# Optimization experiments

Measured on AMD Instinct MI355X. Metric: run time of the kernel, lower is better.

The kernel has to match this reference:

```python
import jax, jax.numpy as jnp
import numpy as np

V, D, B, S = 32000, 1024, 4, 2048
EPS = 1e-12  # matches torch F.normalize eps


def setup_inputs() -> dict:
    key = jax.random.key(0)
    k1, k2, k3 = jax.random.split(key, 3)
    init_embed = jax.random.normal(k1, (V, D), dtype=jnp.float32)
    scale = np.sqrt(D).astype(np.float32)  # default scale = sqrt(embed_dim)
    norm = jnp.maximum(jnp.linalg.norm(init_embed, axis=-1, keepdims=True), EPS)
    in_weight = scale * (init_embed / norm)            # [V, D]
    out_weight = init_embed.T                          # [D, V]
    inputs = jax.random.randint(k2, (B, S), 0, V)      # token ids
    embeds = jax.random.normal(k3, (B, S, D), dtype=jnp.float32)
    return {"inputs": inputs, "embeds": embeds, "in_weight": in_weight, "out_weight": out_weight}


def reference(inputs, embeds, in_weight, out_weight):
    # embed(): one_hot @ in_weight is mathematically an index gather
    embedded = jnp.take(in_weight, inputs, axis=0)          # [B, S, D]
    # unembed(): dense matmul against transposed embedding table
    logits = jnp.einsum('bsd,dv->bsv', embeds, out_weight)  # [B, S, V]
    return embedded, logits
```

## Files before the change

kernel.cpp:

```cpp
#include <hip/hip_runtime.h>
#include <hip/hip_bf16.h>
#include <stdint.h>

#define V_SZ 32000
#define D_SZ 1024
#define M_SZ 8192

typedef __attribute__((ext_vector_type(8))) short bf16x8;
typedef __attribute__((ext_vector_type(4))) float f32x4;
typedef __attribute__((ext_vector_type(16))) float f32x16;

static __device__ __forceinline__ unsigned short f32_to_bf16_rne(float f) {
    union { float f; uint32_t u; } v; v.f = f;
    uint32_t u = v.u;
    uint32_t lsb = (u >> 16) & 1;
    u += 0x7fffu + lsb;
    return (unsigned short)(u >> 16);
}

__global__ void gather_rows(const int* __restrict__ ids,
                            const float* __restrict__ table,
                            float* __restrict__ out) {
    int row = blockIdx.x;
    int id  = ids[row];
    const f32x4* src = (const f32x4*)(table + (size_t)id * D_SZ);
    f32x4*       dst = (f32x4*)(out + (size_t)row * D_SZ);
    __builtin_nontemporal_store(src[threadIdx.x], &dst[threadIdx.x]);
}

__global__ void cast_f32_bf16(const float* __restrict__ in,
                              unsigned short* __restrict__ out, int n8) {
    int i = blockIdx.x * blockDim.x + threadIdx.x;
    int stride = gridDim.x * blockDim.x;
    for (; i < n8; i += stride) {
        const float4* p = (const float4*)(in + (size_t)i * 8);
        float4 a = p[0], b = p[1];
        union { unsigned short s[8]; uint4 v; } r;
        r.s[0] = f32_to_bf16_rne(a.x); r.s[1] = f32_to_bf16_rne(a.y);
        r.s[2] = f32_to_bf16_rne(a.z); r.s[3] = f32_to_bf16_rne(a.w);
        r.s[4] = f32_to_bf16_rne(b.x); r.s[5] = f32_to_bf16_rne(b.y);
        r.s[6] = f32_to_bf16_rne(b.z); r.s[7] = f32_to_bf16_rne(b.w);
        ((uint4*)out)[i] = r.v;
    }
}

__global__ void transpose_cast(const float* __restrict__ w,
                               unsigned short* __restrict__ bt) {
    __shared__ unsigned short tile[32][34];
    int n0 = blockIdx.x * 32;
    int k0 = blockIdx.y * 32;
    int r = threadIdx.x >> 5;
    int c = threadIdx.x & 31;
#pragma unroll
    for (int rr = 0; rr < 32; rr += 8) {
        float v = w[(size_t)(k0 + r + rr) * V_SZ + (n0 + c)];
        tile[c][r + rr] = f32_to_bf16_rne(v);
    }
    __syncthreads();
    int nl = threadIdx.x >> 3;
    int ks = threadIdx.x & 7;
    union { unsigned short s[4]; uint2 v; } r2;
#pragma unroll
    for (int j = 0; j < 4; ++j) r2.s[j] = tile[nl][ks * 4 + j];
    ((uint2*)(bt + (size_t)(n0 + nl) * D_SZ + k0))[ks] = r2.v;
}

#define BM 256
#define BN 256
#define BK 64
#define NSTEP (D_SZ / BK)

static __device__ __forceinline__ void gload_lds16(const unsigned short* g, void* lds) {
    __builtin_amdgcn_global_load_lds(
        (const __attribute__((address_space(1))) void*)g,
        (__attribute__((address_space(3))) void*)lds,
        16, 0, 0);
}

__global__ __launch_bounds__(512, 2)
void gemm_persist(const unsigned short* __restrict__ A,
                  const unsigned short* __restrict__ Bt,
                  float* __restrict__ C) {
    __shared__ __align__(16) char lds[131072];

    const int tid  = threadIdx.x;
    const int lane = tid & 63;
    const int w    = tid >> 6;
    const int wr   = w >> 2;
    const int wc   = w & 3;

    const int bid = blockIdx.x;
    const int xcd = bid & 7;
    const int jb  = bid >> 3;
    const int bm0 = (xcd * 4 + (jb & 3)) * BM;
    const int q0  = jb >> 2;
    const int ntiles = (bid < 160) ? 16 : 15;

    const int hi0  = tid >> 7;
    const int row0 = tid & 127;
    const int dstO = hi0 * 2048 + row0 * 16;
    const unsigned short* gA  = A  + (size_t)(bm0 + row0) * D_SZ + hi0 * 8;
    const unsigned short* gA1 = gA + (size_t)128 * D_SZ;
    const unsigned short* gBc = Bt + (size_t)(q0 * BN + row0) * D_SZ + hi0 * 8;
    const size_t bn_stride = (size_t)8 * BN * D_SZ;

#define STG(ptr, slotbase) do { \
    gload_lds16((ptr),      (char*)lds + (slotbase) + dstO); \
    gload_lds16((ptr) + 32, (char*)lds + (slotbase) + dstO + 8192); } while (0)

    STG(gBc,                           32768);
    STG(gBc + (size_t)128 * D_SZ,      32768 + 16384);
    STG(gA,                            0);
    STG(gA1,                           16384);
    STG(gBc + 64,                      65536 + 32768);
    STG(gBc + (size_t)128 * D_SZ + 64, 65536 + 32768 + 16384);
    STG(gA + 64,                       65536);
    asm volatile("s_waitcnt vmcnt(6)" ::: "memory");
    __builtin_amdgcn_s_barrier();

    f32x16 acc[4][2];
#pragma unroll
    for (int m = 0; m < 4; ++m)
#pragma unroll
        for (int n = 0; n < 2; ++n)
#pragma unroll
            for (int e = 0; e < 16; ++e) acc[m][n][e] = 0.0f;

    bf16x8 a[2][4];
    bf16x8 b[2][4];

    const int base_f = (lane >> 5) * 2048 + (lane & 31) * 16;

#define LDA(mi2, kk, QM) (*(const bf16x8*)(abuf + (kk) * 4096 + ((QM) * 2 + (mi2)) * 512 + base_f))
#define LDB(ni, kk)      (*(const bf16x8*)(bbuf + (kk) * 4096 + (ni) * 512 + base_f))

#define MFMA_Q(QM, QN) \
    __builtin_amdgcn_s_setprio(1); \
    _Pragma("unroll") for (int kk = 0; kk < 4; ++kk) \
    _Pragma("unroll") for (int mi2 = 0; mi2 < 2; ++mi2) \
        acc[(QM) * 2 + mi2][QN] = __builtin_amdgcn_mfma_f32_32x32x16_bf16( \
            a[mi2][kk], b[QN][kk], acc[(QM) * 2 + mi2][QN], 0, 0, 0); \
    __builtin_amdgcn_s_setprio(0);

#define MIDSYNC \
    __builtin_amdgcn_sched_barrier(0); \
    __builtin_amdgcn_s_barrier();

    const int crow = bm0 + wr * 128 + (lane >> 5) * 4;
    const int ccol_f = wc * 64 + (lane & 31);

    for (int r = 0; r < ntiles; ++r) {
        const unsigned short* gBn = gBc + bn_stride;
        const bool last = (r == ntiles - 1);

        for (int t = 0; t < NSTEP; ++t) {
            const int   dbuf = (t & 1) << 16;
            const char* abuf = (const char*)lds + dbuf + wr * 16384;
            const char* bbuf = (const char*)lds + dbuf + 32768
                               + (wc >> 1) * 16384 + (wc & 1) * 1024;
            const int nslot = (dbuf ^ 65536);

            a[0][0] = LDA(0, 0, 0); a[0][1] = LDA(0, 1, 0);
            a[0][2] = LDA(0, 2, 0); a[0][3] = LDA(0, 3, 0);
            a[1][0] = LDA(1, 0, 0); a[1][1] = LDA(1, 1, 0);
            a[1][2] = LDA(1, 2, 0); a[1][3] = LDA(1, 3, 0);
            b[0][0] = LDB(0, 0); b[0][1] = LDB(0, 1);
            b[0][2] = LDB(0, 2); b[0][3] = LDB(0, 3);
            if (!(last && t == 15)) STG(gA1 + ((t + 1) & 15) * 64, nslot + 16384);
            MIDSYNC;
            MFMA_Q(0, 0);
            __builtin_amdgcn_s_barrier();

            b[1][0] = LDB(1, 0); b[1][1] = LDB(1, 1);
            b[1][2] = LDB(1, 2); b[1][3] = LDB(1, 3);
            MIDSYNC;
            MFMA_Q(0, 1);
            __builtin_amdgcn_s_barrier();

            a[0][0] = LDA(0, 0, 1); a[0][1] = LDA(0, 1, 1);
            a[0][2] = LDA(0, 2, 1); a[0][3] = LDA(0, 3, 1);
            a[1][0] = LDA(1, 0, 1); a[1][1] = LDA(1, 1, 1);
            a[1][2] = LDA(1, 2, 1); a[1][3] = LDA(1, 3, 1);
            if (t < 14 || !last) {
                const unsigned short* pb = (t < 14) ? gBc + (t + 2) * 64
                                                    : gBn + (t - 14) * 64;
                STG(pb, dbuf + 32768);
            }
            MIDSYNC;
            MFMA_Q(1, 1);
            __builtin_amdgcn_s_barrier();

            if (t < 14 || !last) {
                const unsigned short* pb = (t < 14) ? gBc + (t + 2) * 64
                                                    : gBn + (t - 14) * 64;
                STG(pb + (size_t)128 * D_SZ, dbuf + 32768 + 16384);
                STG(gA + ((t + 2) & 15) * 64, dbuf);
            }
            MFMA_Q(1, 0);
            if (last && t >= 14) { asm volatile("s_waitcnt vmcnt(0)" ::: "memory"); }
            else                 { asm volatile("s_waitcnt vmcnt(6)" ::: "memory"); }
            __builtin_amdgcn_s_barrier();
        }

        const int ccol = (q0 + 8 * r) * BN + ccol_f;
#pragma unroll
        for (int mi = 0; mi < 4; ++mi)
#pragma unroll
            for (int ni = 0; ni < 2; ++ni) {
                float* base = C + (size_t)(crow + mi * 32) * V_SZ + (ccol + ni * 32);
#pragma unroll
                for (int e = 0; e < 16; ++e) {
                    int roff = (e & 3) + 8 * (e >> 2);
                    base[(size_t)roff * V_SZ] = acc[mi][ni][e];
                }
            }
#pragma unroll
        for (int m = 0; m < 4; ++m)
#pragma unroll
            for (int n = 0; n < 2; ++n)
#pragma unroll
                for (int e = 0; e < 16; ++e) acc[m][n][e] = 0.0f;

        gBc = gBn;
    }
#undef STG
#undef LDA
#undef LDB
#undef MFMA_Q
#undef MIDSYNC
}

extern "C" void kernel_launch(void* const* d_in, const int* in_sizes, int n_in,
                              void* d_out, int out_size, void* d_ws, size_t ws_size,
                              hipStream_t stream) {
    const int*   ids        = (const int*)d_in[0];
    const float* embeds     = (const float*)d_in[1];
    const float* in_weight  = (const float*)d_in[2];
    const float* out_weight = (const float*)d_in[3];

    float* out_embedded = (float*)d_out;
    float* out_logits   = (float*)d_out + (size_t)M_SZ * D_SZ;

    unsigned short* Abf  = (unsigned short*)d_ws;
    unsigned short* Btbf = Abf + (size_t)M_SZ * D_SZ;

    gather_rows<<<M_SZ, 256, 0, stream>>>(ids, in_weight, out_embedded);
    cast_f32_bf16<<<2048, 256, 0, stream>>>(embeds, Abf, M_SZ * D_SZ / 8);
    transpose_cast<<<dim3(V_SZ / 32, D_SZ / 32), 256, 0, stream>>>(out_weight, Btbf);
    gemm_persist<<<dim3(256), 512, 0, stream>>>(Abf, Btbf, out_logits);
}
```

Before: 774.0 us.

## Deepen prefetch of A-tile halves and use nontemporal stores for logits

The second A half-tile is now prefetched two k-steps ahead together with the other loads, rather than one step ahead inside the first phase. The prologue is reordered to issue both k-slices up front, and the wait counts are relaxed to vmcnt(8), with a special vmcnt(63) case at the first step of each new tile. Output logit stores become nontemporal so the large C write does not pollute the caches. The risks are a subtle race from the changed wait accounting and more in-flight loads per wave.

```diff
diff --git a/kernel.cpp b/kernel.cpp
--- a/kernel.cpp
+++ b/kernel.cpp
@@ -108,14 +108,15 @@
     gload_lds16((ptr),      (char*)lds + (slotbase) + dstO); \
     gload_lds16((ptr) + 32, (char*)lds + (slotbase) + dstO + 8192); } while (0)
 
-    STG(gBc,                           32768);
-    STG(gBc + (size_t)128 * D_SZ,      32768 + 16384);
     STG(gA,                            0);
     STG(gA1,                           16384);
+    STG(gBc,                           32768);
+    STG(gBc + (size_t)128 * D_SZ,      49152);
+    STG(gA + 64,                       65536);
+    STG(gA1 + 64,                      65536 + 16384);
     STG(gBc + 64,                      65536 + 32768);
-    STG(gBc + (size_t)128 * D_SZ + 64, 65536 + 32768 + 16384);
-    STG(gA + 64,                       65536);
-    asm volatile("s_waitcnt vmcnt(6)" ::: "memory");
+    STG(gBc + (size_t)128 * D_SZ + 64, 65536 + 49152);
+    asm volatile("s_waitcnt vmcnt(8)" ::: "memory");
     __builtin_amdgcn_s_barrier();
 
     f32x16 acc[4][2];
@@ -158,7 +159,11 @@
             const char* abuf = (const char*)lds + dbuf + wr * 16384;
             const char* bbuf = (const char*)lds + dbuf + 32768
                                + (wc >> 1) * 16384 + (wc & 1) * 1024;
-            const int nslot = (dbuf ^ 65536);
+
+            const bool stg = (t < 14) || !last;
+            const unsigned short* pb = (t < 14) ? gBc + (t + 2) * 64
+                                                : gBn + (t - 14) * 64;
+            const int ka2 = ((t + 2) & 15) * 64;
 
             a[0][0] = LDA(0, 0, 0); a[0][1] = LDA(0, 1, 0);
             a[0][2] = LDA(0, 2, 0); a[0][3] = LDA(0, 3, 0);
@@ -166,7 +171,6 @@
             a[1][2] = LDA(1, 2, 0); a[1][3] = LDA(1, 3, 0);
             b[0][0] = LDB(0, 0); b[0][1] = LDB(0, 1);
             b[0][2] = LDB(0, 2); b[0][3] = LDB(0, 3);
-            if (!(last && t == 15)) STG(gA1 + ((t + 1) & 15) * 64, nslot + 16384);
             MIDSYNC;
             MFMA_Q(0, 0);
             __builtin_amdgcn_s_barrier();
@@ -181,24 +185,24 @@
             a[0][2] = LDA(0, 2, 1); a[0][3] = LDA(0, 3, 1);
             a[1][0] = LDA(1, 0, 1); a[1][1] = LDA(1, 1, 1);
             a[1][2] = LDA(1, 2, 1); a[1][3] = LDA(1, 3, 1);
-            if (t < 14 || !last) {
-                const unsigned short* pb = (t < 14) ? gBc + (t + 2) * 64
-                                                    : gBn + (t - 14) * 64;
-                STG(pb, dbuf + 32768);
-            }
+            if (stg) STG(pb, dbuf + 32768);
             MIDSYNC;
             MFMA_Q(1, 1);
             __builtin_amdgcn_s_barrier();
 
-            if (t < 14 || !last) {
-                const unsigned short* pb = (t < 14) ? gBc + (t + 2) * 64
-                                                    : gBn + (t - 14) * 64;
-                STG(pb + (size_t)128 * D_SZ, dbuf + 32768 + 16384);
-                STG(gA + ((t + 2) & 15) * 64, dbuf);
+            if (stg) {
+                STG(pb + (size_t)128 * D_SZ, dbuf + 49152);
+                STG(gA  + ka2, dbuf);
+                STG(gA1 + ka2, dbuf + 16384);
             }
             MFMA_Q(1, 0);
-            if (last && t >= 14) { asm volatile("s_waitcnt vmcnt(0)" ::: "memory"); }
-            else                 { asm volatile("s_waitcnt vmcnt(6)" ::: "memory"); }
+            if (last && t >= 14) {
+                asm volatile("s_waitcnt vmcnt(0)" ::: "memory");
+            } else if (t == 0 && r > 0) {
+                asm volatile("s_waitcnt vmcnt(63)" ::: "memory");
+            } else {
+                asm volatile("s_waitcnt vmcnt(8)" ::: "memory");
+            }
             __builtin_amdgcn_s_barrier();
         }
 
@@ -211,7 +215,7 @@
 #pragma unroll
                 for (int e = 0; e < 16; ++e) {
                     int roff = (e & 3) + 8 * (e >> 2);
-                    base[(size_t)roff * V_SZ] = acc[mi][ni][e];
+                    __builtin_nontemporal_store(acc[mi][ni][e], base + (size_t)roff * V_SZ);
                 }
             }
 #pragma unroll
```

Measured after the change: 770.3 us. Within noise of the previous version (-0.5%).
